# Performance work log

Hardware: AMD Instinct MI355X
Metric: run time of the kernel (lower is better)

## Reference

```python
import jax, jax.numpy as jnp
import numpy as np

B, S, I, O, H = 128, 256, 512, 512, 1024


def setup_inputs() -> dict:
    key = jax.random.key(0)
    ks = jax.random.split(key, 8)
    sH = 1.0 / np.sqrt(H)
    sI = 1.0 / np.sqrt(I + O)
    y = jax.random.normal(ks[0], (B, S, I), dtype=jnp.float32)
    # groundTruth is a one-hot token sequence (teacher forcing targets)
    gt_idx = jax.random.randint(ks[1], (B, S), 0, O)
    groundTruth = jax.nn.one_hot(gt_idx, O, dtype=jnp.float32)
    hx = jnp.zeros((B, H), dtype=jnp.float32)
    weight_ih = jax.random.normal(ks[2], (3 * H, I + O), dtype=jnp.float32) * sI
    bias_ih = jax.random.normal(ks[3], (3 * H,), dtype=jnp.float32) * sI
    weight_hh = jax.random.normal(ks[4], (3 * H, H), dtype=jnp.float32) * sH
    bias_hh = jax.random.normal(ks[5], (3 * H,), dtype=jnp.float32) * sH
    lin_w = jax.random.normal(ks[6], (O, H), dtype=jnp.float32) * sH
    lin_b = jax.random.normal(ks[7], (O,), dtype=jnp.float32) * sH
    gotoken = jnp.zeros((1, O), dtype=jnp.float32).at[0, 0].set(1.0)
    return {"y": y, "groundTruth": groundTruth, "hx": hx,
            "weight_ih": weight_ih, "bias_ih": bias_ih,
            "weight_hh": weight_hh, "bias_hh": bias_hh,
            "lin_w": lin_w, "lin_b": lin_b, "gotoken": gotoken}


def reference(y, groundTruth, hx, weight_ih, bias_ih, weight_hh, bias_hh, lin_w, lin_b, gotoken):
    b, s, _ = y.shape
    o = lin_b.shape[0]
    # Teacher forcing: target at step i is gotoken for i=0, else groundTruth[:, i-1]
    tgt0 = jnp.broadcast_to(gotoken[None, :, :], (b, 1, o))
    targets = jnp.concatenate([tgt0, groundTruth[:, :-1, :]], axis=1)      # [B,S,O]
    inputs = jnp.concatenate([y, targets], axis=-1)                        # [B,S,I+O]
    # Input-side gate projections have no recurrence -> one big GEMM up front
    gi_all = jnp.einsum('bsi,gi->sbg', inputs, weight_ih) + bias_ih        # [S,B,3H]

    def step(h, gi_t):
        gh = h @ weight_hh.T + bias_hh                                     # [B,3H]
        i_r, i_z, i_n = jnp.split(gi_t, 3, axis=-1)
        h_r, h_z, h_n = jnp.split(gh, 3, axis=-1)
        resetgate = jax.nn.sigmoid(i_r + h_r)
        inputgate = jax.nn.sigmoid(i_z + h_z)
        pre = i_n + resetgate * h_n
        newgate = jnp.tanh(pre)
        hy = newgate + inputgate * (h - newgate)
        return hy, (hy, pre)

    hx_final, (hs, pres) = jax.lax.scan(step, hx, gi_all)
    hs = jnp.swapaxes(hs, 0, 1)                                            # [B,S,H]
    preactivation = jnp.swapaxes(pres, 0, 1)                               # [B,S,H]
    logp = jax.nn.log_softmax(jnp.einsum('bsh,oh->bso', hs, lin_w) + lin_b, axis=-1)
    probs = jnp.exp(logp)                                                  # [B,S,O]
    # probabilistic_sampling=False -> topk(.,1) indices -> one-hot
    sampled_output = jax.nn.one_hot(jnp.argmax(probs, axis=-1), o, dtype=probs.dtype)
    return probs, preactivation, sampled_output, hx_final
```

## Files before the change

kernel.cpp:

```cpp
#include <hip/hip_runtime.h>
#include <hip/hip_bf16.h>

typedef short bf16x8 __attribute__((ext_vector_type(8)));
typedef float f32x4  __attribute__((ext_vector_type(4)));

#define NB   128
#define NS   256
#define NI   512
#define NO   512
#define NH   1024
#define G3   3072

__device__ inline unsigned short f2bf(float f) {
    unsigned u = __builtin_bit_cast(unsigned, f);
    u += 0x7fffu + ((u >> 16) & 1u);
    return (unsigned short)(u >> 16);
}
__device__ inline float bf2f(unsigned short h) {
    unsigned u = ((unsigned)h) << 16;
    return __builtin_bit_cast(float, u);
}
__device__ inline bf16x8 as_bf8(uint4 u) { return __builtin_bit_cast(bf16x8, u); }
__device__ inline void split3(float x, unsigned short& h1, unsigned short& h2, unsigned short& h3) {
    h1 = f2bf(x); float r1 = x - bf2f(h1);
    h2 = f2bf(r1); float r2 = r1 - bf2f(h2);
    h3 = f2bf(r2);
}

#define MF(acc, A_, B_) acc = __builtin_amdgcn_mfma_f32_16x16x32_bf16(A_, B_, acc, 0, 0, 0)

__global__ void k_tidx(const float* __restrict__ gt, const float* __restrict__ gotok,
                       int* __restrict__ tidx) {
    int m    = blockIdx.x * 4 + (threadIdx.x >> 6);
    int lane = threadIdx.x & 63;
    int s = m >> 7, b = m & 127;
    const float* src = (s == 0) ? gotok : gt + ((size_t)b * NS + (s - 1)) * NO;
    int idx = 0x7fffffff;
    for (int j = lane; j < NO; j += 64)
        if (src[j] > 0.5f) idx = min(idx, j);
    for (int off = 32; off; off >>= 1) idx = min(idx, __shfl_down(idx, off));
    if (lane == 0) tidx[m] = idx;
}

__global__ void k_split3(const float* __restrict__ in, unsigned short* __restrict__ o1,
                         unsigned short* __restrict__ o2, unsigned short* __restrict__ o3, int n) {
    int i = blockIdx.x * blockDim.x + threadIdx.x;
    if (i < n) { unsigned short a, b, c; split3(in[i], a, b, c); o1[i] = a; o2[i] = b; o3[i] = c; }
}
__global__ void k_split3I(const float* __restrict__ wih, unsigned short* __restrict__ o1,
                          unsigned short* __restrict__ o2, unsigned short* __restrict__ o3) {
    int i = blockIdx.x * blockDim.x + threadIdx.x;
    int g = i >> 9, k = i & 511;
    unsigned short a, b, c; split3(wih[(size_t)g * (NI + NO) + k], a, b, c);
    o1[i] = a; o2[i] = b; o3[i] = c;
}
__global__ void k_wot(const float* __restrict__ w_ih, float* __restrict__ wOT) {
    int g = blockIdx.x * 256 + threadIdx.x;
    int t = blockIdx.y;
    wOT[(size_t)t * G3 + g] = w_ih[(size_t)g * (NI + NO) + NI + t];
}
__global__ void k_h0(const float* __restrict__ hx, float* __restrict__ hF,
                     unsigned short* __restrict__ r1, unsigned short* __restrict__ r2,
                     unsigned short* __restrict__ r3) {
    int i = blockIdx.x * blockDim.x + threadIdx.x;
    float v = hx[i];
    hF[i] = v;
    unsigned short a, b, c; split3(v, a, b, c);
    r1[15 * 131072 + i] = a; r2[15 * 131072 + i] = b; r3[15 * 131072 + i] = c;
}

__global__ __launch_bounds__(512) void k_gi16(
    const unsigned short* __restrict__ wi1, const unsigned short* __restrict__ wi2,
    const unsigned short* __restrict__ wi3,
    const float* __restrict__ y, const float* __restrict__ wOT,
    const float* __restrict__ b_ih, const float* __restrict__ b_hh,
    const int* __restrict__ tidx,
    float* __restrict__ giRZ, float* __restrict__ pre_out, int base) {
    int bid = blockIdx.x;
    int rg = bid & 15, cg = bid >> 4;
    int tid = threadIdx.x, lane = tid & 63, wave = tid >> 6;
    int col = lane & 15, quad = lane >> 4;
    int s = base + rg;
    int arow = wave * 16 + col;
    f32x4 acc[12] = {};
    const float* Yp = y + ((size_t)arow * NS + s) * NI + quad * 8;
    const uint4* B1 = (const uint4*)wi1 + (size_t)(cg * 192 + col) * 64 + quad;
    const uint4* B2 = (const uint4*)wi2 + (size_t)(cg * 192 + col) * 64 + quad;
    const uint4* B3 = (const uint4*)wi3 + (size_t)(cg * 192 + col) * 64 + quad;
    #pragma unroll 1
    for (int kk = 0; kk < 16; kk++) {
        float4 f0 = *(const float4*)(Yp + kk * 32);
        float4 f1 = *(const float4*)(Yp + kk * 32 + 4);
        float v[8] = {f0.x, f0.y, f0.z, f0.w, f1.x, f1.y, f1.z, f1.w};
        bf16x8 a1, a2, a3;
        #pragma unroll
        for (int e = 0; e < 8; e++) {
            unsigned short u1, u2, u3; split3(v[e], u1, u2, u3);
            a1[e] = (short)u1; a2[e] = (short)u2; a3[e] = (short)u3;
        }
        #pragma unroll
        for (int t = 0; t < 12; t++) {
            bf16x8 b1 = as_bf8(B1[t * 1024 + kk * 4]);
            bf16x8 b2 = as_bf8(B2[t * 1024 + kk * 4]);
            bf16x8 b3 = as_bf8(B3[t * 1024 + kk * 4]);
            MF(acc[t], a1, b1); MF(acc[t], a1, b2); MF(acc[t], a2, b1);
            MF(acc[t], a1, b3); MF(acc[t], a3, b1); MF(acc[t], a2, b2);
        }
    }
    int ti[4];
    #pragma unroll
    for (int r = 0; r < 4; r++) ti[r] = tidx[s * 128 + wave * 16 + quad * 4 + r];
    #pragma unroll
    for (int t = 0; t < 12; t++) {
        int cg3 = cg * 192 + t * 16 + col;
        int g = cg3 >> 10, cc = cg3 & 1023;
        float bi = b_ih[cg3] + (g < 2 ? b_hh[cg3] : 0.f);
        #pragma unroll
        for (int r = 0; r < 4; r++) {
            int b = wave * 16 + quad * 4 + r;
            float val = acc[t][r] + wOT[(size_t)ti[r] * G3 + cg3] + bi;
            if (g == 2) pre_out[((size_t)b * NS + s) * NH + cc] = val;
            else        giRZ[((((size_t)rg * 2 + g) * 128 + b) << 10) + cc] = val;
        }
    }
}

__global__ __launch_bounds__(512) void k_step(
    const unsigned short* __restrict__ rh1, const unsigned short* __restrict__ rh2,
    const unsigned short* __restrict__ rh3,
    const unsigned short* __restrict__ wh1, const unsigned short* __restrict__ wh2,
    const unsigned short* __restrict__ wh3,
    const float* __restrict__ b_hh,
    const float* __restrict__ giRZ,
    float* __restrict__ hF,
    unsigned short* __restrict__ oh1, unsigned short* __restrict__ oh2,
    unsigned short* __restrict__ oh3,
    float* __restrict__ pre_out, int s) {
    __shared__ f32x4 lred[3][2][3][64];
    int bid = blockIdx.x;
    int c_tile = ((bid & 7) << 3) | ((bid >> 3) & 7);
    int mt = bid >> 6;
    int tid = threadIdx.x, lane = tid & 63, wave = tid >> 6;
    int rowhalf = wave & 1, kq = wave >> 1;
    int col = lane & 15, quad = lane >> 4;
    int m0 = mt * 32 + rowhalf * 16;
    int c0 = c_tile * 16;
    int p = (s + 15) & 15, q = s & 15;
    f32x4 ar = {}, az = {}, anh = {};

    float g_r[4], g_z[4], p_in[4], p_h[4];
    float bhn = 0.f;
    if (kq == 0) {
        int c = c0 + col;
        bhn = b_hh[2 * NH + c];
        #pragma unroll
        for (int r = 0; r < 4; r++) {
            int b = m0 + quad * 4 + r;
            g_r[r]  = giRZ[(((size_t)q * 2 + 0) * 128 + b) * 1024 + c];
            g_z[r]  = giRZ[(((size_t)q * 2 + 1) * 128 + b) * 1024 + c];
            p_in[r] = pre_out[((size_t)b * NS + s) * NH + c];
            p_h[r]  = hF[(size_t)b * NH + c];
        }
    }

    const uint4* A1 = (const uint4*)rh1 + (size_t)p * 16384 + (size_t)(m0 + col) * 128 + kq * 32 + quad;
    const uint4* A2 = (const uint4*)rh2 + (size_t)p * 16384 + (size_t)(m0 + col) * 128 + kq * 32 + quad;
    const uint4* A3 = (const uint4*)rh3 + (size_t)p * 16384 + (size_t)(m0 + col) * 128 + kq * 32 + quad;
    const uint4* B1 = (const uint4*)wh1 + (size_t)(c0 + col) * 128 + kq * 32 + quad;
    const uint4* B2 = (const uint4*)wh2 + (size_t)(c0 + col) * 128 + kq * 32 + quad;
    const uint4* B3 = (const uint4*)wh3 + (size_t)(c0 + col) * 128 + kq * 32 + quad;
    #pragma unroll 2
    for (int kk = 0; kk < 8; kk++) {
        bf16x8 a1 = as_bf8(A1[kk * 4]), a2 = as_bf8(A2[kk * 4]), a3 = as_bf8(A3[kk * 4]);
        {
            bf16x8 b1 = as_bf8(B1[kk * 4]), b2 = as_bf8(B2[kk * 4]), b3 = as_bf8(B3[kk * 4]);
            MF(ar, a1, b1); MF(ar, a1, b2); MF(ar, a2, b1);
            MF(ar, a1, b3); MF(ar, a3, b1); MF(ar, a2, b2);
        }
        {
            bf16x8 b1 = as_bf8(B1[kk * 4 + 131072]), b2 = as_bf8(B2[kk * 4 + 131072]), b3 = as_bf8(B3[kk * 4 + 131072]);
            MF(az, a1, b1); MF(az, a1, b2); MF(az, a2, b1);
            MF(az, a1, b3); MF(az, a3, b1); MF(az, a2, b2);
        }
        {
            bf16x8 b1 = as_bf8(B1[kk * 4 + 262144]), b2 = as_bf8(B2[kk * 4 + 262144]), b3 = as_bf8(B3[kk * 4 + 262144]);
            MF(anh, a1, b1); MF(anh, a1, b2); MF(anh, a2, b1);
            MF(anh, a1, b3); MF(anh, a3, b1); MF(anh, a2, b2);
        }
    }
    if (kq) {
        lred[kq - 1][rowhalf][0][lane] = ar;
        lred[kq - 1][rowhalf][1][lane] = az;
        lred[kq - 1][rowhalf][2][lane] = anh;
    }
    __syncthreads();
    if (kq == 0) {
        #pragma unroll
        for (int j = 0; j < 3; j++) {
            ar  += lred[j][rowhalf][0][lane];
            az  += lred[j][rowhalf][1][lane];
            anh += lred[j][rowhalf][2][lane];
        }
        int c = c0 + col;
        #pragma unroll
        for (int r = 0; r < 4; r++) {
            int b = m0 + quad * 4 + r;
            float sr = ar[r] + g_r[r];
            float sz = az[r] + g_z[r];
            float rg = 1.f / (1.f + expf(-sr));
            float zg = 1.f / (1.f + expf(-sz));
            float hn_ = anh[r] + bhn;
            float pre = p_in[r] + rg * hn_;
            float ng = tanhf(pre);
            float hy = ng + zg * (p_h[r] - ng);
            hF[(size_t)b * NH + c] = hy;
            pre_out[((size_t)b * NS + s) * NH + c] = pre;
            unsigned short u1, u2, u3; split3(hy, u1, u2, u3);
            size_t ro = (size_t)q * 131072 + (size_t)b * NH + c;
            oh1[ro] = u1; oh2[ro] = u2; oh3[ro] = u3;
        }
    }
}

__global__ __launch_bounds__(256) void k_logits16(
    const unsigned short* __restrict__ rh1, const unsigned short* __restrict__ rh2,
    const unsigned short* __restrict__ rh3,
    const unsigned short* __restrict__ lw1, const unsigned short* __restrict__ lw2,
    const unsigned short* __restrict__ lw3,
    const float* __restrict__ lin_b,
    float* __restrict__ probs, int* __restrict__ amax, int base) {
    __shared__ __align__(16) float lt[16 * 512];
    __shared__ float red[16 * 16];
    __shared__ int  redi[16 * 16];
    __shared__ float rmax[16], rsum[16];
    __shared__ int  ridx[16];
    int slot = blockIdx.x >> 3, b0 = (blockIdx.x & 7) * 16;
    int s = base + slot;
    int tid = threadIdx.x, lane = tid & 63, wave = tid >> 6;
    int col = lane & 15, quad = lane >> 4;
    f32x4 acc[8] = {};
    const uint4* A1 = (const uint4*)rh1 + (size_t)slot * 16384 + (size_t)(b0 + col) * 128 + quad;
    const uint4* A2 = (const uint4*)rh2 + (size_t)slot * 16384 + (size_t)(b0 + col) * 128 + quad;
    const uint4* A3 = (const uint4*)rh3 + (size_t)slot * 16384 + (size_t)(b0 + col) * 128 + quad;
    const uint4* B1 = (const uint4*)lw1 + (size_t)(wave * 128 + col) * 128 + quad;
    const uint4* B2 = (const uint4*)lw2 + (size_t)(wave * 128 + col) * 128 + quad;
    const uint4* B3 = (const uint4*)lw3 + (size_t)(wave * 128 + col) * 128 + quad;
    for (int kk = 0; kk < 32; kk++) {
        bf16x8 a1 = as_bf8(A1[kk * 4]), a2 = as_bf8(A2[kk * 4]), a3 = as_bf8(A3[kk * 4]);
        #pragma unroll
        for (int t = 0; t < 8; t++) {
            bf16x8 b1 = as_bf8(B1[kk * 4 + t * 2048]);
            bf16x8 b2 = as_bf8(B2[kk * 4 + t * 2048]);
            bf16x8 b3 = as_bf8(B3[kk * 4 + t * 2048]);
            MF(acc[t], a1, b1); MF(acc[t], a1, b2); MF(acc[t], a2, b1);
            MF(acc[t], a1, b3); MF(acc[t], a3, b1); MF(acc[t], a2, b2);
        }
    }
    #pragma unroll
    for (int t = 0; t < 8; t++) {
        int n = wave * 128 + t * 16 + col;
        float lb = lin_b[n];
        #pragma unroll
        for (int r = 0; r < 4; r++)
            lt[(quad * 4 + r) * 512 + n] = acc[t][r] + lb;
    }
    __syncthreads();
    int r = tid >> 4, t16 = tid & 15;
    const float* row = lt + r * 512 + t16 * 32;
    float mx = row[0];
    for (int j = 1; j < 32; j++) mx = fmaxf(mx, row[j]);
    red[r * 16 + t16] = mx;
    __syncthreads();
    if (t16 == 0) {
        float m2 = red[r * 16];
        for (int j = 1; j < 16; j++) m2 = fmaxf(m2, red[r * 16 + j]);
        rmax[r] = m2;
    }
    __syncthreads();
    float RM = rmax[r];
    float sum = 0.f; int ai = 0x7fffffff;
    for (int j = 0; j < 32; j++) {
        float v = row[j];
        sum += expf(v - RM);
        if (v == RM) ai = min(ai, t16 * 32 + j);
    }
    red[r * 16 + t16] = sum; redi[r * 16 + t16] = ai;
    __syncthreads();
    if (t16 == 0) {
        float s2 = 0.f; int i2 = 0x7fffffff;
        for (int j = 0; j < 16; j++) { s2 += red[r * 16 + j]; i2 = min(i2, redi[r * 16 + j]); }
        rsum[r] = s2; ridx[r] = i2;
    }
    __syncthreads();
    float inv = 1.f / rsum[r];
    int b = b0 + r;
    size_t off = ((size_t)b * NS + s) * NO + t16 * 32;
    for (int j = 0; j < 32; j++)
        probs[off + j] = expf(row[j] - RM) * inv;
    if (t16 == 0) amax[s * 128 + b] = ridx[r];
}

__global__ void k_samp(const int* __restrict__ amax, float* __restrict__ samp) {
    int m = blockIdx.x;
    int b = m & 127, s = m >> 7;
    int ai = amax[m];
    size_t off = ((size_t)b * NS + s) * NO;
    for (int j = threadIdx.x; j < NO; j += 256)
        samp[off + j] = (j == ai) ? 1.f : 0.f;
}

extern "C" void kernel_launch(void* const* d_in, const int* in_sizes, int n_in,
                              void* d_out, int out_size, void* d_ws, size_t ws_size,
                              hipStream_t stream) {
    const float* y     = (const float*)d_in[0];
    const float* gt    = (const float*)d_in[1];
    const float* hx    = (const float*)d_in[2];
    const float* w_ih  = (const float*)d_in[3];
    const float* b_ih  = (const float*)d_in[4];
    const float* w_hh  = (const float*)d_in[5];
    const float* b_hh  = (const float*)d_in[6];
    const float* lw    = (const float*)d_in[7];
    const float* lb    = (const float*)d_in[8];
    const float* gotok = (const float*)d_in[9];

    char* ws = (char*)d_ws;
    unsigned short* wh1 = (unsigned short*)(ws);
    unsigned short* wh2 = (unsigned short*)(ws + 6291456ull);
    unsigned short* wh3 = (unsigned short*)(ws + 12582912ull);
    unsigned short* wi1 = (unsigned short*)(ws + 18874368ull);
    unsigned short* wi2 = (unsigned short*)(ws + 22020096ull);
    unsigned short* wi3 = (unsigned short*)(ws + 25165824ull);
    unsigned short* lw1 = (unsigned short*)(ws + 28311552ull);
    unsigned short* lw2 = (unsigned short*)(ws + 29360128ull);
    unsigned short* lw3 = (unsigned short*)(ws + 30408704ull);
    unsigned short* rh1 = (unsigned short*)(ws + 31457280ull);
    unsigned short* rh2 = (unsigned short*)(ws + 35651584ull);
    unsigned short* rh3 = (unsigned short*)(ws + 39845888ull);
    float*          hF  = (float*)(ws + 44040192ull);
    int*            tidx= (int*)(ws + 44564480ull);
    int*            amax= (int*)(ws + 44695552ull);

    float* out   = (float*)d_out;
    float* probs = out;
    float* pre   = out + 16777216;
    float* samp  = out + 50331648;
    float* hxf   = out + 67108864;

    float* giRZ = samp;
    float* wOT  = samp + 4194304;

    k_tidx<<<8192, 256, 0, stream>>>(gt, gotok, tidx);
    k_split3<<<12288, 256, 0, stream>>>(w_hh, wh1, wh2, wh3, 3145728);
    k_split3I<<<6144, 256, 0, stream>>>(w_ih, wi1, wi2, wi3);
    k_split3<<<2048, 256, 0, stream>>>(lw, lw1, lw2, lw3, 524288);
    k_h0<<<512, 256, 0, stream>>>(hx, hF, rh1, rh2, rh3);
    k_wot<<<dim3(12, 512), 256, 0, stream>>>(w_ih, wOT);

    k_gi16<<<256, 512, 0, stream>>>(wi1, wi2, wi3, y, wOT, b_ih, b_hh, tidx,
                                    giRZ, pre, 0);
    for (int s = 0; s < NS; s++) {
        k_step<<<256, 512, 0, stream>>>(rh1, rh2, rh3, wh1, wh2, wh3,
                                        b_hh, giRZ, hF, rh1, rh2, rh3, pre, s);
        if ((s & 15) == 15) {
            if (s < NS - 1)
                k_gi16<<<256, 512, 0, stream>>>(wi1, wi2, wi3, y, wOT, b_ih, b_hh, tidx,
                                                giRZ, pre, s + 1);
            k_logits16<<<128, 256, 0, stream>>>(rh1, rh2, rh3, lw1, lw2, lw3, lb,
                                                probs, amax, s - 15);
        }
    }

    k_samp<<<32768, 256, 0, stream>>>(amax, samp);
    hipMemcpyAsync(hxf, hF, 524288, hipMemcpyDeviceToDevice, stream);
}
```

Before: 11.25 ms.

## Replace per-step kernel launches with a persistent cooperative kernel using grid syncs

Merges the input projection, recurrent step and logits/softmax kernels into one persistent cooperative kernel of 256 blocks that loops over all timesteps, using grid.sync between phases in place of roughly 290 separate launches. The logits phase now runs on 128 blocks of 512 threads, each wave covering 64 output columns. The other 128 blocks run the next chunk's input projection at the same time, two tiles per block. This removes launch overhead and lets the logits and input-projection work overlap, at the cost of grid-wide barrier latency and the larger shared-memory and register footprint of the merged kernel.

New measurement: 19.17 ms. 1.7x slower.

```diff
diff --git a/kernel.cpp b/kernel.cpp
--- a/kernel.cpp
+++ b/kernel.cpp
@@ -1,5 +1,7 @@
 #include <hip/hip_runtime.h>
 #include <hip/hip_bf16.h>
+#include <hip/hip_cooperative_groups.h>
+namespace cg = cooperative_groups;
 
 typedef short bf16x8 __attribute__((ext_vector_type(8)));
 typedef float f32x4  __attribute__((ext_vector_type(4)));
@@ -69,24 +71,31 @@
     r1[15 * 131072 + i] = a; r2[15 * 131072 + i] = b; r3[15 * 131072 + i] = c;
 }
 
-__global__ __launch_bounds__(512) void k_gi16(
-    const unsigned short* __restrict__ wi1, const unsigned short* __restrict__ wi2,
-    const unsigned short* __restrict__ wi3,
-    const float* __restrict__ y, const float* __restrict__ wOT,
-    const float* __restrict__ b_ih, const float* __restrict__ b_hh,
-    const int* __restrict__ tidx,
-    float* __restrict__ giRZ, float* __restrict__ pre_out, int base) {
-    int bid = blockIdx.x;
-    int rg = bid & 15, cg = bid >> 4;
+struct GruArgs {
+    const unsigned short *wh1, *wh2, *wh3;
+    const unsigned short *wi1, *wi2, *wi3;
+    const unsigned short *lw1, *lw2, *lw3;
+    unsigned short *rh1, *rh2, *rh3;
+    const float *y, *wOT, *b_ih, *b_hh, *lin_b;
+    const int *tidx;
+    float *giRZ;
+    float *hF;
+    float *pre;
+    float *probs;
+    int *amax;
+};
+
+__device__ __forceinline__ void gi_phase(const GruArgs& a, int vbid, int base) {
+    int rg = vbid & 15, cg = vbid >> 4;
     int tid = threadIdx.x, lane = tid & 63, wave = tid >> 6;
     int col = lane & 15, quad = lane >> 4;
     int s = base + rg;
     int arow = wave * 16 + col;
     f32x4 acc[12] = {};
-    const float* Yp = y + ((size_t)arow * NS + s) * NI + quad * 8;
-    const uint4* B1 = (const uint4*)wi1 + (size_t)(cg * 192 + col) * 64 + quad;
-    const uint4* B2 = (const uint4*)wi2 + (size_t)(cg * 192 + col) * 64 + quad;
-    const uint4* B3 = (const uint4*)wi3 + (size_t)(cg * 192 + col) * 64 + quad;
+    const float* Yp = a.y + ((size_t)arow * NS + s) * NI + quad * 8;
+    const uint4* B1 = (const uint4*)a.wi1 + (size_t)(cg * 192 + col) * 64 + quad;
+    const uint4* B2 = (const uint4*)a.wi2 + (size_t)(cg * 192 + col) * 64 + quad;
+    const uint4* B3 = (const uint4*)a.wi3 + (size_t)(cg * 192 + col) * 64 + quad;
     #pragma unroll 1
     for (int kk = 0; kk < 16; kk++) {
         float4 f0 = *(const float4*)(Yp + kk * 32);
@@ -109,35 +118,24 @@
     }
     int ti[4];
     #pragma unroll
-    for (int r = 0; r < 4; r++) ti[r] = tidx[s * 128 + wave * 16 + quad * 4 + r];
+    for (int r = 0; r < 4; r++) ti[r] = a.tidx[s * 128 + wave * 16 + quad * 4 + r];
     #pragma unroll
     for (int t = 0; t < 12; t++) {
         int cg3 = cg * 192 + t * 16 + col;
         int g = cg3 >> 10, cc = cg3 & 1023;
-        float bi = b_ih[cg3] + (g < 2 ? b_hh[cg3] : 0.f);
+        float bi = a.b_ih[cg3] + (g < 2 ? a.b_hh[cg3] : 0.f);
         #pragma unroll
         for (int r = 0; r < 4; r++) {
             int b = wave * 16 + quad * 4 + r;
-            float val = acc[t][r] + wOT[(size_t)ti[r] * G3 + cg3] + bi;
-            if (g == 2) pre_out[((size_t)b * NS + s) * NH + cc] = val;
-            else        giRZ[((((size_t)rg * 2 + g) * 128 + b) << 10) + cc] = val;
-        }
-    }
-}
-
-__global__ __launch_bounds__(512) void k_step(
-    const unsigned short* __restrict__ rh1, const unsigned short* __restrict__ rh2,
-    const unsigned short* __restrict__ rh3,
-    const unsigned short* __restrict__ wh1, const unsigned short* __restrict__ wh2,
-    const unsigned short* __restrict__ wh3,
-    const float* __restrict__ b_hh,
-    const float* __restrict__ giRZ,
-    float* __restrict__ hF,
-    unsigned short* __restrict__ oh1, unsigned short* __restrict__ oh2,
-    unsigned short* __restrict__ oh3,
-    float* __restrict__ pre_out, int s) {
-    __shared__ f32x4 lred[3][2][3][64];
-    int bid = blockIdx.x;
+            float val = acc[t][r] + a.wOT[(size_t)ti[r] * G3 + cg3] + bi;
+            if (g == 2) a.pre[((size_t)b * NS + s) * NH + cc] = val;
+            else        a.giRZ[((((size_t)rg * 2 + g) * 128 + b) << 10) + cc] = val;
+        }
+    }
+}
+
+__device__ __forceinline__ void step_phase(const GruArgs& a, int bid, int s,
+                                           f32x4 (*lred)[2][3][64]) {
     int c_tile = ((bid & 7) << 3) | ((bid >> 3) & 7);
     int mt = bid >> 6;
     int tid = threadIdx.x, lane = tid & 63, wave = tid >> 6;
@@ -152,23 +150,23 @@
     float bhn = 0.f;
     if (kq == 0) {
         int c = c0 + col;
-        bhn = b_hh[2 * NH + c];
+        bhn = a.b_hh[2 * NH + c];
         #pragma unroll
         for (int r = 0; r < 4; r++) {
             int b = m0 + quad * 4 + r;
-            g_r[r]  = giRZ[(((size_t)q * 2 + 0) * 128 + b) * 1024 + c];
-            g_z[r]  = giRZ[(((size_t)q * 2 + 1) * 128 + b) * 1024 + c];
-            p_in[r] = pre_out[((size_t)b * NS + s) * NH + c];
-            p_h[r]  = hF[(size_t)b * NH + c];
-        }
-    }
-
-    const uint4* A1 = (const uint4*)rh1 + (size_t)p * 16384 + (size_t)(m0 + col) * 128 + kq * 32 + quad;
-    const uint4* A2 = (const uint4*)rh2 + (size_t)p * 16384 + (size_t)(m0 + col) * 128 + kq * 32 + quad;
-    const uint4* A3 = (const uint4*)rh3 + (size_t)p * 16384 + (size_t)(m0 + col) * 128 + kq * 32 + quad;
-    const uint4* B1 = (const uint4*)wh1 + (size_t)(c0 + col) * 128 + kq * 32 + quad;
-    const uint4* B2 = (const uint4*)wh2 + (size_t)(c0 + col) * 128 + kq * 32 + quad;
-    const uint4* B3 = (const uint4*)wh3 + (size_t)(c0 + col) * 128 + kq * 32 + quad;
+            g_r[r]  = a.giRZ[(((size_t)q * 2 + 0) * 128 + b) * 1024 + c];
+            g_z[r]  = a.giRZ[(((size_t)q * 2 + 1) * 128 + b) * 1024 + c];
+            p_in[r] = a.pre[((size_t)b * NS + s) * NH + c];
+            p_h[r]  = a.hF[(size_t)b * NH + c];
+        }
+    }
+
+    const uint4* A1 = (const uint4*)a.rh1 + (size_t)p * 16384 + (size_t)(m0 + col) * 128 + kq * 32 + quad;
+    const uint4* A2 = (const uint4*)a.rh2 + (size_t)p * 16384 + (size_t)(m0 + col) * 128 + kq * 32 + quad;
+    const uint4* A3 = (const uint4*)a.rh3 + (size_t)p * 16384 + (size_t)(m0 + col) * 128 + kq * 32 + quad;
+    const uint4* B1 = (const uint4*)a.wh1 + (size_t)(c0 + col) * 128 + kq * 32 + quad;
+    const uint4* B2 = (const uint4*)a.wh2 + (size_t)(c0 + col) * 128 + kq * 32 + quad;
+    const uint4* B3 = (const uint4*)a.wh3 + (size_t)(c0 + col) * 128 + kq * 32 + quad;
     #pragma unroll 2
     for (int kk = 0; kk < 8; kk++) {
         bf16x8 a1 = as_bf8(A1[kk * 4]), a2 = as_bf8(A2[kk * 4]), a3 = as_bf8(A3[kk * 4]);
@@ -213,42 +211,32 @@
             float pre = p_in[r] + rg * hn_;
             float ng = tanhf(pre);
             float hy = ng + zg * (p_h[r] - ng);
-            hF[(size_t)b * NH + c] = hy;
-            pre_out[((size_t)b * NS + s) * NH + c] = pre;
+            a.hF[(size_t)b * NH + c] = hy;
+            a.pre[((size_t)b * NS + s) * NH + c] = pre;
             unsigned short u1, u2, u3; split3(hy, u1, u2, u3);
             size_t ro = (size_t)q * 131072 + (size_t)b * NH + c;
-            oh1[ro] = u1; oh2[ro] = u2; oh3[ro] = u3;
-        }
-    }
-}
-
-__global__ __launch_bounds__(256) void k_logits16(
-    const unsigned short* __restrict__ rh1, const unsigned short* __restrict__ rh2,
-    const unsigned short* __restrict__ rh3,
-    const unsigned short* __restrict__ lw1, const unsigned short* __restrict__ lw2,
-    const unsigned short* __restrict__ lw3,
-    const float* __restrict__ lin_b,
-    float* __restrict__ probs, int* __restrict__ amax, int base) {
-    __shared__ __align__(16) float lt[16 * 512];
-    __shared__ float red[16 * 16];
-    __shared__ int  redi[16 * 16];
-    __shared__ float rmax[16], rsum[16];
-    __shared__ int  ridx[16];
-    int slot = blockIdx.x >> 3, b0 = (blockIdx.x & 7) * 16;
+            a.rh1[ro] = u1; a.rh2[ro] = u2; a.rh3[ro] = u3;
+        }
+    }
+}
+
+__device__ __forceinline__ void logits_phase(const GruArgs& a, int bid, int base,
+        float* lt, float* red, int* redi, float* rmax, float* rsum, int* ridx) {
+    int slot = bid >> 3, b0 = (bid & 7) * 16;
     int s = base + slot;
     int tid = threadIdx.x, lane = tid & 63, wave = tid >> 6;
     int col = lane & 15, quad = lane >> 4;
-    f32x4 acc[8] = {};
-    const uint4* A1 = (const uint4*)rh1 + (size_t)slot * 16384 + (size_t)(b0 + col) * 128 + quad;
-    const uint4* A2 = (const uint4*)rh2 + (size_t)slot * 16384 + (size_t)(b0 + col) * 128 + quad;
-    const uint4* A3 = (const uint4*)rh3 + (size_t)slot * 16384 + (size_t)(b0 + col) * 128 + quad;
-    const uint4* B1 = (const uint4*)lw1 + (size_t)(wave * 128 + col) * 128 + quad;
-    const uint4* B2 = (const uint4*)lw2 + (size_t)(wave * 128 + col) * 128 + quad;
-    const uint4* B3 = (const uint4*)lw3 + (size_t)(wave * 128 + col) * 128 + quad;
+    f32x4 acc[4] = {};
+    const uint4* A1 = (const uint4*)a.rh1 + (size_t)slot * 16384 + (size_t)(b0 + col) * 128 + quad;
+    const uint4* A2 = (const uint4*)a.rh2 + (size_t)slot * 16384 + (size_t)(b0 + col) * 128 + quad;
+    const uint4* A3 = (const uint4*)a.rh3 + (size_t)slot * 16384 + (size_t)(b0 + col) * 128 + quad;
+    const uint4* B1 = (const uint4*)a.lw1 + (size_t)(wave * 64 + col) * 128 + quad;
+    const uint4* B2 = (const uint4*)a.lw2 + (size_t)(wave * 64 + col) * 128 + quad;
+    const uint4* B3 = (const uint4*)a.lw3 + (size_t)(wave * 64 + col) * 128 + quad;
     for (int kk = 0; kk < 32; kk++) {
         bf16x8 a1 = as_bf8(A1[kk * 4]), a2 = as_bf8(A2[kk * 4]), a3 = as_bf8(A3[kk * 4]);
         #pragma unroll
-        for (int t = 0; t < 8; t++) {
+        for (int t = 0; t < 4; t++) {
             bf16x8 b1 = as_bf8(B1[kk * 4 + t * 2048]);
             bf16x8 b2 = as_bf8(B2[kk * 4 + t * 2048]);
             bf16x8 b3 = as_bf8(B3[kk * 4 + t * 2048]);
@@ -257,47 +245,74 @@
         }
     }
     #pragma unroll
-    for (int t = 0; t < 8; t++) {
-        int n = wave * 128 + t * 16 + col;
-        float lb = lin_b[n];
+    for (int t = 0; t < 4; t++) {
+        int n = wave * 64 + t * 16 + col;
+        float lb = a.lin_b[n];
         #pragma unroll
         for (int r = 0; r < 4; r++)
             lt[(quad * 4 + r) * 512 + n] = acc[t][r] + lb;
     }
     __syncthreads();
-    int r = tid >> 4, t16 = tid & 15;
-    const float* row = lt + r * 512 + t16 * 32;
+    int r = tid >> 5, t32 = tid & 31;
+    const float* row = lt + r * 512 + t32 * 16;
     float mx = row[0];
-    for (int j = 1; j < 32; j++) mx = fmaxf(mx, row[j]);
-    red[r * 16 + t16] = mx;
-    __syncthreads();
-    if (t16 == 0) {
-        float m2 = red[r * 16];
-        for (int j = 1; j < 16; j++) m2 = fmaxf(m2, red[r * 16 + j]);
+    for (int j = 1; j < 16; j++) mx = fmaxf(mx, row[j]);
+    red[r * 32 + t32] = mx;
+    __syncthreads();
+    if (t32 == 0) {
+        float m2 = red[r * 32];
+        for (int j = 1; j < 32; j++) m2 = fmaxf(m2, red[r * 32 + j]);
         rmax[r] = m2;
     }
     __syncthreads();
     float RM = rmax[r];
     float sum = 0.f; int ai = 0x7fffffff;
-    for (int j = 0; j < 32; j++) {
+    for (int j = 0; j < 16; j++) {
         float v = row[j];
         sum += expf(v - RM);
-        if (v == RM) ai = min(ai, t16 * 32 + j);
-    }
-    red[r * 16 + t16] = sum; redi[r * 16 + t16] = ai;
-    __syncthreads();
-    if (t16 == 0) {
+        if (v == RM) ai = min(ai, t32 * 16 + j);
+    }
+    red[r * 32 + t32] = sum; redi[r * 32 + t32] = ai;
+    __syncthreads();
+    if (t32 == 0) {
         float s2 = 0.f; int i2 = 0x7fffffff;
-        for (int j = 0; j < 16; j++) { s2 += red[r * 16 + j]; i2 = min(i2, redi[r * 16 + j]); }
+        for (int j = 0; j < 32; j++) { s2 += red[r * 32 + j]; i2 = min(i2, redi[r * 32 + j]); }
         rsum[r] = s2; ridx[r] = i2;
     }
     __syncthreads();
     float inv = 1.f / rsum[r];
     int b = b0 + r;
-    size_t off = ((size_t)b * NS + s) * NO + t16 * 32;
-    for (int j = 0; j < 32; j++)
-        probs[off + j] = expf(row[j] - RM) * inv;
-    if (t16 == 0) amax[s * 128 + b] = ridx[r];
+    size_t off = ((size_t)b * NS + s) * NO + t32 * 16;
+    for (int j = 0; j < 16; j++)
+        a.probs[off + j] = expf(row[j] - RM) * inv;
+    if (t32 == 0) a.amax[s * 128 + b] = ridx[r];
+}
+
+__global__ __launch_bounds__(512, 2) void k_gru(GruArgs a) {
+    cg::grid_group grid = cg::this_grid();
+    __shared__ f32x4 lred[3][2][3][64];
+    __shared__ __align__(16) float lt[16 * 512];
+    __shared__ float red[16 * 32];
+    __shared__ int  redi[16 * 32];
+    __shared__ float rmax[16], rsum[16];
+    __shared__ int  ridx[16];
+    int bid = blockIdx.x;
+
+    gi_phase(a, bid, 0);
+    grid.sync();
+    for (int s = 0; s < NS; s++) {
+        step_phase(a, bid, s, lred);
+        grid.sync();
+        if ((s & 15) == 15) {
+            if (bid < 128) {
+                logits_phase(a, bid, s - 15, lt, red, redi, rmax, rsum, ridx);
+            } else if (s < NS - 1) {
+                gi_phase(a, ((bid - 128) << 1) | 0, s + 1);
+                gi_phase(a, ((bid - 128) << 1) | 1, s + 1);
+            }
+            grid.sync();
+        }
+    }
 }
 
 __global__ void k_samp(const int* __restrict__ amax, float* __restrict__ samp) {
@@ -356,19 +371,16 @@
     k_h0<<<512, 256, 0, stream>>>(hx, hF, rh1, rh2, rh3);
     k_wot<<<dim3(12, 512), 256, 0, stream>>>(w_ih, wOT);
 
-    k_gi16<<<256, 512, 0, stream>>>(wi1, wi2, wi3, y, wOT, b_ih, b_hh, tidx,
-                                    giRZ, pre, 0);
-    for (int s = 0; s < NS; s++) {
-        k_step<<<256, 512, 0, stream>>>(rh1, rh2, rh3, wh1, wh2, wh3,
-                                        b_hh, giRZ, hF, rh1, rh2, rh3, pre, s);
-        if ((s & 15) == 15) {
-            if (s < NS - 1)
-                k_gi16<<<256, 512, 0, stream>>>(wi1, wi2, wi3, y, wOT, b_ih, b_hh, tidx,
-                                                giRZ, pre, s + 1);
-            k_logits16<<<128, 256, 0, stream>>>(rh1, rh2, rh3, lw1, lw2, lw3, lb,
-                                                probs, amax, s - 15);
-        }
-    }
+    GruArgs ga;
+    ga.wh1 = wh1; ga.wh2 = wh2; ga.wh3 = wh3;
+    ga.wi1 = wi1; ga.wi2 = wi2; ga.wi3 = wi3;
+    ga.lw1 = lw1; ga.lw2 = lw2; ga.lw3 = lw3;
+    ga.rh1 = rh1; ga.rh2 = rh2; ga.rh3 = rh3;
+    ga.y = y; ga.wOT = wOT; ga.b_ih = b_ih; ga.b_hh = b_hh; ga.lin_b = lb;
+    ga.tidx = tidx; ga.giRZ = giRZ; ga.hF = hF; ga.pre = pre;
+    ga.probs = probs; ga.amax = amax;
+    void* kp[] = { (void*)&ga };
+    hipLaunchCooperativeKernel((const void*)k_gru, dim3(256), dim3(512), kp, 0, stream);
 
     k_samp<<<32768, 256, 0, stream>>>(amax, samp);
     hipMemcpyAsync(hxf, hF, 524288, hipMemcpyDeviceToDevice, stream);
```
